# Optimization experiments

Measured on AMD Instinct MI355X. Metric: run time of the kernel, lower is better.

The kernel has to match this reference:

```python
import jax, jax.numpy as jnp
import numpy as np

EMBED = 1024
HEADS = 16
HEAD_DIM = EMBED // HEADS


def setup_inputs() -> dict:
    key = jax.random.key(0)
    ks = jax.random.split(key, 12)
    B, S, E = 2, 2048, EMBED
    scale = 1.0 / np.sqrt(E)
    inp = {
        "query": jax.random.normal(ks[0], (B, S, E), jnp.float32),
        "key": jax.random.normal(ks[1], (B, S, E), jnp.float32),
        "value": jax.random.normal(ks[2], (B, S, E), jnp.float32),
        "Wq": jax.random.normal(ks[3], (E, E), jnp.float32) * scale,
        "bq": jax.random.normal(ks[4], (E,), jnp.float32) * 0.01,
        "Wk": jax.random.normal(ks[5], (E, E), jnp.float32) * scale,
        "bk": jax.random.normal(ks[6], (E,), jnp.float32) * 0.01,
        "Wv": jax.random.normal(ks[7], (E, E), jnp.float32) * scale,
        "bv": jax.random.normal(ks[8], (E,), jnp.float32) * 0.01,
        "Wo": jax.random.normal(ks[9], (E, E), jnp.float32) * scale,
        "bo": jax.random.normal(ks[10], (E,), jnp.float32) * 0.01,
    }
    return inp


def reference(query, key, value, Wq, bq, Wk, bk, Wv, bv, Wo, bo):
    B, Sq, E = query.shape
    Sk = key.shape[1]
    H, D = HEADS, HEAD_DIM
    # QKV projections (torch Linear: x @ W.T + b)
    q = (query @ Wq.T + bq).reshape(B, Sq, H, D)
    k = (key @ Wk.T + bk).reshape(B, Sk, H, D)
    v = (value @ Wv.T + bv).reshape(B, Sk, H, D)
    # energy: [B, H, Sq, Sk]; note scale = 1/sqrt(embed_size), not head_dim
    energy = jnp.einsum("bqhd,bkhd->bhqk", q, k)
    scale = jnp.asarray(E, energy.dtype) ** 0.5
    attn = jax.nn.softmax(energy / scale, axis=-1)
    out = jnp.einsum("bhqk,bkhd->bqhd", attn, v).reshape(B, Sq, E)
    # fc_out (dropout is identity at eval)
    return out @ Wo.T + bo
```

## Files before the change

### kernel.cpp

```cpp
#include <hip/hip_runtime.h>
#include <hip/hip_bf16.h>

typedef __hip_bfloat16 bf16;
typedef short frag8 __attribute__((ext_vector_type(8)));
typedef _Float16 half4 __attribute__((ext_vector_type(4)));
typedef _Float16 half8 __attribute__((ext_vector_type(8)));
typedef __fp16 fp16x2 __attribute__((ext_vector_type(2)));
typedef float f32x4 __attribute__((ext_vector_type(4)));

typedef __attribute__((address_space(3))) void lds_void;
typedef __attribute__((address_space(1))) const void gbl_void;

__device__ __forceinline__ void gld16(const void* g, void* l) {
  __builtin_amdgcn_global_load_lds((gbl_void*)g, (lds_void*)l, 16, 0, 0);
}

__device__ __forceinline__ unsigned short f2bf(float f) {
  union { float f; unsigned u; } x; x.f = f;
  unsigned r = x.u + 0x7FFFu + ((x.u >> 16) & 1u);
  return (unsigned short)(r >> 16);
}

#define QSCALE 0.0450842200278f
#define MFIX 4.0f

struct CvtArgs {
  const float4* src[7];
  ushort4* dst[7];
  int n4[7];
};
__global__ __launch_bounds__(256) void cvt_all(CvtArgs a) {
  const int t = blockIdx.y;
  const int i = blockIdx.x * 256 + threadIdx.x;
  if (i >= a.n4[t]) return;
  float4 v = a.src[t][i];
  ushort4 o;
  o.x = f2bf(v.x); o.y = f2bf(v.y); o.z = f2bf(v.z); o.w = f2bf(v.w);
  a.dst[t][i] = o;
}

__device__ __forceinline__ void mfma32(f32x4 (&acc)[8][4], const frag8 (&a8)[8], const frag8 (&b4)[4]) {
  __builtin_amdgcn_s_setprio(1);
  #pragma unroll
  for (int i = 0; i < 8; ++i) {
    #pragma unroll
    for (int j = 0; j < 4; ++j)
      acc[i][j] = __builtin_amdgcn_mfma_f32_16x16x32_bf16(a8[i], b4[j], acc[i][j], 0, 0, 0);
  }
  __builtin_amdgcn_s_setprio(0);
}

__global__ __launch_bounds__(512, 2)
void gemm_qkv256(const bf16* __restrict__ A0, const bf16* __restrict__ A1, const bf16* __restrict__ A2,
                 const bf16* __restrict__ W0, const bf16* __restrict__ W1, const bf16* __restrict__ W2,
                 const float* __restrict__ b0, const float* __restrict__ b1, const float* __restrict__ b2,
                 void* __restrict__ o0, void* __restrict__ o1, void* __restrict__ o2) {
  __shared__ __align__(16) char smem[131072];
  bf16* As = (bf16*)smem;
  bf16* Bs = (bf16*)(smem + 65536);
  const int tid = threadIdx.x;
  const int wave = tid >> 6, lane = tid & 63, quad = lane >> 4, l16 = lane & 15;
  const int wm = wave >> 2, wn = wave & 3;
  const int bn = blockIdx.x, bm = blockIdx.y, z = blockIdx.z;

  const bf16* A = A0; const bf16* W = W0; const float* bias = b0; void* out = o0;
  if (z == 1) { A = A1; W = W1; bias = b1; out = o1; }
  else if (z == 2) { A = A2; W = W2; bias = b2; out = o2; }

  const bf16* Ab = A + (size_t)bm * 256 * 1024;
  const bf16* Wb = W + (size_t)bn * 256 * 1024;
  const int c0_ = tid & 3, r0_ = tid >> 2;
  const int gcp = ((c0_ ^ ((r0_ >> 1) & 3)) << 3);
  const int rc2 = (quad ^ ((l16 >> 1) & 3)) << 3;

  auto stageA = [&](int kt, bf16* dst) {
    #pragma unroll
    for (int is = 0; is < 2; ++is) {
      const int r = r0_ + is * 128;
      gld16(Ab + (size_t)r * 1024 + kt * 32 + gcp, (void*)(dst + (is * 512 + tid) * 8));
    }
  };
  auto stageW = [&](int kt, bf16* dst) {
    #pragma unroll
    for (int is = 0; is < 2; ++is) {
      const int r = r0_ + is * 128;
      gld16(Wb + (size_t)r * 1024 + kt * 32 + gcp, (void*)(dst + (is * 512 + tid) * 8));
    }
  };
  auto ldsA8 = [&](const bf16* ah, frag8 (&a8)[8]) {
    #pragma unroll
    for (int i = 0; i < 8; ++i)
      a8[i] = *(const frag8*)&ah[(wm * 128 + i * 16 + l16) * 32 + rc2];
  };
  auto ldsB4 = [&](const bf16* bh, frag8 (&b4)[4]) {
    #pragma unroll
    for (int j = 0; j < 4; ++j)
      b4[j] = *(const frag8*)&bh[(wn * 64 + j * 16 + l16) * 32 + rc2];
  };

  f32x4 acc[8][4];
  #pragma unroll
  for (int i = 0; i < 8; ++i)
    #pragma unroll
    for (int j = 0; j < 4; ++j)
      acc[i][j] = (f32x4){0.f, 0.f, 0.f, 0.f};

  stageA(0, As + 0 * 8192); stageW(0, Bs + 0 * 8192);
  stageA(1, As + 1 * 8192); stageW(1, Bs + 1 * 8192);
  stageA(2, As + 2 * 8192); stageW(2, Bs + 2 * 8192);

  #pragma unroll 4
  for (int t = 0; t < 28; ++t) {
    asm volatile("s_waitcnt vmcnt(8)" ::: "memory");
    __builtin_amdgcn_s_barrier();
    const bf16* ab = As + (t & 3) * 8192;
    const bf16* bb = Bs + (t & 3) * 8192;
    frag8 a8[8], b4[4];
    ldsA8(ab, a8); ldsB4(bb, b4);
    stageA(t + 3, As + ((t + 3) & 3) * 8192);
    stageW(t + 3, Bs + ((t + 3) & 3) * 8192);
    asm volatile("s_waitcnt lgkmcnt(0)" ::: "memory");
    mfma32(acc, a8, b4);
  }
  {
    asm volatile("s_waitcnt vmcnt(8)" ::: "memory");
    __builtin_amdgcn_s_barrier();
    frag8 a8[8], b4[4];
    ldsA8(As + 0 * 8192, a8); ldsB4(Bs + 0 * 8192, b4);
    stageA(31, As + 3 * 8192);
    stageW(31, Bs + 3 * 8192);
    asm volatile("s_waitcnt lgkmcnt(0)" ::: "memory");
    mfma32(acc, a8, b4);
  }
  {
    asm volatile("s_waitcnt vmcnt(8)" ::: "memory");
    __builtin_amdgcn_s_barrier();
    frag8 a8[8], b4[4];
    ldsA8(As + 1 * 8192, a8); ldsB4(Bs + 1 * 8192, b4);
    asm volatile("s_waitcnt lgkmcnt(0)" ::: "memory");
    mfma32(acc, a8, b4);
  }
  {
    asm volatile("s_waitcnt vmcnt(4)" ::: "memory");
    __builtin_amdgcn_s_barrier();
    frag8 a8[8], b4[4];
    ldsA8(As + 2 * 8192, a8); ldsB4(Bs + 2 * 8192, b4);
    asm volatile("s_waitcnt lgkmcnt(0)" ::: "memory");
    mfma32(acc, a8, b4);
  }
  {
    asm volatile("s_waitcnt vmcnt(0)" ::: "memory");
    __builtin_amdgcn_s_barrier();
    frag8 a8[8], b4[4];
    ldsA8(As + 3 * 8192, a8); ldsB4(Bs + 3 * 8192, b4);
    asm volatile("s_waitcnt lgkmcnt(0)" ::: "memory");
    mfma32(acc, a8, b4);
  }

  if (z == 2) {
    _Float16* vlds = (_Float16*)smem;
    __builtin_amdgcn_s_barrier();
    #pragma unroll
    for (int j = 0; j < 4; ++j) {
      const int col = bn * 256 + wn * 64 + j * 16 + l16;
      const float bv = bias[col];
      const int d = j * 16 + l16;
      #pragma unroll
      for (int i = 0; i < 8; ++i) {
        const int g = wm * 2 + (i >> 2);
        const int kb = (i & 3) * 16 + quad * 4;
        half4 h;
        #pragma unroll
        for (int r = 0; r < 4; ++r)
          h[r] = (_Float16)(acc[i][j][r] + bv);
        const int off = ((wn * 4 + g) << 12) + d * 64 + ((((kb >> 3) ^ (d & 7)) << 3)) + (kb & 7);
        *(half4*)&vlds[off] = h;
      }
    }
    __builtin_amdgcn_s_barrier();
    const int b_ = bm >> 3;
    #pragma unroll
    for (int rd = 0; rd < 16; ++rd) {
      const int l = rd * 4096 + tid * 8;
      const int wnp = l >> 14, g = (l >> 12) & 3, off = l & 4095;
      const size_t bhp = (size_t)(b_ * 16 + bn * 4 + wnp);
      const size_t addr = bhp * 131072 + (size_t)((bm & 7) * 4 + g) * 4096 + (size_t)off;
      *(uint4*)&((_Float16*)out)[addr] = *(const uint4*)&vlds[l];
    }
  } else {
    #pragma unroll
    for (int j = 0; j < 4; ++j) {
      const int col = bn * 256 + wn * 64 + j * 16 + l16;
      const float bv = bias[col];
      #pragma unroll
      for (int i = 0; i < 8; ++i) {
        #pragma unroll
        for (int r = 0; r < 4; ++r) {
          const int row = bm * 256 + wm * 128 + i * 16 + quad * 4 + r;
          float v = acc[i][j][r] + bv;
          const int b = row >> 11, s = row & 2047;
          const int hh = col >> 6, d = col & 63;
          const size_t bh = (size_t)(b * 16 + hh);
          if (z == 0) {
            v *= QSCALE;
            ((bf16*)out)[(bh * 2048 + s) * 64 + d] = __float2bfloat16(v);
          } else {
            const int g = s >> 6, l32 = s & 31, G32 = (s >> 5) & 1;
            const int q_ = (l32 >> 3) & 3, t_ = (l32 >> 2) & 1, i_ = l32 & 3;
            const int r64 = G32 * 32 + t_ * 16 + q_ * 4 + i_;
            const size_t addr = bh * 131072 + (size_t)g * 4096 + (size_t)r64 * 64
                              + (size_t)(((d >> 3) ^ (r64 & 7)) << 3) + (d & 7);
            ((bf16*)out)[addr] = __float2bfloat16(v);
          }
        }
      }
    }
  }
}

template<int MODE>
__global__ __launch_bounds__(256)
void gemm_bt(const bf16* __restrict__ A0, const bf16* __restrict__ A1, const bf16* __restrict__ A2,
             const bf16* __restrict__ W0, const bf16* __restrict__ W1, const bf16* __restrict__ W2,
             const float* __restrict__ b0, const float* __restrict__ b1, const float* __restrict__ b2,
             void* __restrict__ o0, void* __restrict__ o1, void* __restrict__ o2) {
  constexpr int NK = 1024;
  constexpr int BN = (MODE == 1) ? 128 : 64;
  __shared__ __align__(16) bf16 As[2][128 * 32];
  __shared__ __align__(16) bf16 Bs[2][BN * 32];
  const int tid = threadIdx.x;
  const int wave = tid >> 6, lane = tid & 63, quad = lane >> 4, l16 = lane & 15;
  const int wm = wave >> 1, wn = wave & 1;
  const int bn = blockIdx.x, bm = blockIdx.y;

  const bf16* A = A0; const bf16* W = W0; const float* bias = b0; void* out = o0;

  const bf16* Ab = A + (size_t)bm * 128 * NK;
  const bf16* Wb = W + (size_t)bn * BN * NK;
  const int c0_ = tid & 3, r0_ = tid >> 2;
  const int rc = (quad ^ (l16 & 3)) << 3;

  auto stageA = [&](int k0, int buf) {
    #pragma unroll
    for (int is = 0; is < 2; ++is) {
      const int c = tid + is * 256;
      const int r = r0_ + is * 64;
      const int gc = (c0_ ^ (r & 3)) << 3;
      gld16(Ab + (size_t)r * NK + k0 + gc, (void*)(&As[buf][(size_t)c * 8]));
    }
  };
  auto stageW = [&](int k0, int buf) {
    const int r = r0_;
    const int gc = (c0_ ^ (r & 3)) << 3;
    gld16(Wb + (size_t)r * NK + k0 + gc, (void*)(&Bs[buf][(size_t)tid * 8]));
  };

  f32x4 acc[4][2];
  #pragma unroll
  for (int i = 0; i < 4; ++i)
    #pragma unroll
    for (int j = 0; j < 2; ++j)
      acc[i][j] = (f32x4){0.f, 0.f, 0.f, 0.f};

  stageA(0, 0); stageW(0, 0);
  #pragma unroll 2
  for (int kt = 0; kt < 32; ++kt) {
    __syncthreads();
    if (kt < 31) { stageA((kt + 1) * 32, (kt + 1) & 1); stageW((kt + 1) * 32, (kt + 1) & 1); }
    const bf16* as_ = As[kt & 1];
    const bf16* bs_ = Bs[kt & 1];
    frag8 af[4], bfr[2];
    #pragma unroll
    for (int i = 0; i < 4; ++i)
      af[i] = *(const frag8*)&as_[(wm * 64 + i * 16 + l16) * 32 + rc];
    #pragma unroll
    for (int j = 0; j < 2; ++j)
      bfr[j] = *(const frag8*)&bs_[(wn * 32 + j * 16 + l16) * 32 + rc];
    #pragma unroll
    for (int i = 0; i < 4; ++i)
      #pragma unroll
      for (int j = 0; j < 2; ++j)
        acc[i][j] = __builtin_amdgcn_mfma_f32_16x16x32_bf16(af[i], bfr[j], acc[i][j], 0, 0, 0);
  }

  #pragma unroll
  for (int j = 0; j < 2; ++j) {
    const int col = bn * 64 + wn * 32 + j * 16 + l16;
    const float bv = bias[col];
    #pragma unroll
    for (int i = 0; i < 4; ++i) {
      #pragma unroll
      for (int r = 0; r < 4; ++r) {
        const int row = bm * 128 + wm * 64 + i * 16 + quad * 4 + r;
        ((float*)out)[(size_t)row * 1024 + col] = acc[i][j][r] + bv;
      }
    }
  }
}

__global__ __launch_bounds__(512, 2)
void flash_attn(const bf16* __restrict__ Q, const bf16* __restrict__ K,
                const _Float16* __restrict__ Vt, bf16* __restrict__ ctx) {
  __shared__ __align__(16) char smem[65536];
  bf16* Ks = (bf16*)smem;
  _Float16* Vs = (_Float16*)(smem + 32768);
  const int tid = threadIdx.x;
  const int wave = tid >> 6, lane = tid & 63, quad = lane >> 4, l16 = lane & 15;
  const int qg = wave & 3, kvg = wave >> 2;
  const int bh = blockIdx.x, b = bh >> 4, h = bh & 15;
  const int q0 = blockIdx.y * 256 + qg * 64;
  const bf16* Qb = Q + (size_t)bh * 131072;
  const bf16* Kb = K + (size_t)bh * 131072;
  const _Float16* Vb = Vt + (size_t)bh * 131072;

  frag8 qf[4][2];
  #pragma unroll
  for (int qt = 0; qt < 4; ++qt)
    #pragma unroll
    for (int ks = 0; ks < 2; ++ks)
      qf[qt][ks] = *(const frag8*)(Qb + (size_t)(q0 + qt * 16 + l16) * 64 + ks * 32 + quad * 8);

  f32x4 rsv[4];
  f32x4 o[4][4];
  #pragma unroll
  for (int qt = 0; qt < 4; ++qt) {
    rsv[qt] = (f32x4){0.f, 0.f, 0.f, 0.f};
    #pragma unroll
    for (int dt = 0; dt < 4; ++dt)
      o[qt][dt] = (f32x4){0.f, 0.f, 0.f, 0.f};
  }

  const int xk = l16 & 7;

  auto stage = [&](int kt, int buf) {
    #pragma unroll
    for (int s = 0; s < 2; ++s) {
      const int g = s * 16 + kt;
      gld16(Kb + (size_t)g * 4096 + (size_t)tid * 8, (void*)(Ks + (s * 2 + buf) * 4096 + tid * 8));
      gld16(Vb + (size_t)g * 4096 + (size_t)tid * 8, (void*)(Vs + (s * 2 + buf) * 4096 + tid * 8));
    }
  };

  stage(0, 0);
  #pragma unroll 2
  for (int kt = 0; kt < 16; ++kt) {
    __syncthreads();
    if (kt < 15) stage(kt + 1, (kt + 1) & 1);
    const bf16* ks_ = Ks + (kvg * 2 + (kt & 1)) * 4096;
    const _Float16* vs_ = Vs + (kvg * 2 + (kt & 1)) * 4096;

    f32x4 s[4][4];
    #pragma unroll
    for (int qt = 0; qt < 4; ++qt)
      #pragma unroll
      for (int jt = 0; jt < 4; ++jt)
        s[qt][jt] = (f32x4){-MFIX, -MFIX, -MFIX, -MFIX};
    #pragma unroll
    for (int ks = 0; ks < 2; ++ks) {
      frag8 kf[4];
      #pragma unroll
      for (int jt = 0; jt < 4; ++jt)
        kf[jt] = *(const frag8*)&ks_[(jt * 16 + l16) * 64 + (((ks * 4 + quad) ^ xk) << 3)];
      __builtin_amdgcn_s_setprio(1);
      #pragma unroll
      for (int qt = 0; qt < 4; ++qt)
        #pragma unroll
        for (int jt = 0; jt < 4; ++jt)
          s[qt][jt] = __builtin_amdgcn_mfma_f32_16x16x32_bf16(kf[jt], qf[qt][ks], s[qt][jt], 0, 0, 0);
      __builtin_amdgcn_s_setprio(0);
    }

    half8 pb[4][2];
    #pragma unroll
    for (int qt = 0; qt < 4; ++qt) {
      #pragma unroll
      for (int jt = 0; jt < 4; ++jt) {
        f32x4 p4;
        #pragma unroll
        for (int r = 0; r < 4; ++r)
          p4[r] = __builtin_amdgcn_exp2f(s[qt][jt][r]);
        rsv[qt] += p4;
        union { fp16x2 h2[2]; half4 h4; } u;
        u.h2[0] = __builtin_amdgcn_cvt_pkrtz(p4[0], p4[1]);
        u.h2[1] = __builtin_amdgcn_cvt_pkrtz(p4[2], p4[3]);
        const int jtp = jt >> 1, hi = (jt & 1) * 4;
        pb[qt][jtp][hi + 0] = u.h4[0];
        pb[qt][jtp][hi + 1] = u.h4[1];
        pb[qt][jtp][hi + 2] = u.h4[2];
        pb[qt][jtp][hi + 3] = u.h4[3];
      }
    }

    #pragma unroll
    for (int jtp = 0; jtp < 2; ++jtp) {
      half8 vf[4];
      #pragma unroll
      for (int dt = 0; dt < 4; ++dt)
        vf[dt] = *(const half8*)&vs_[(dt * 16 + l16) * 64 + (((jtp * 4 + quad) ^ xk) << 3)];
      __builtin_amdgcn_s_setprio(1);
      #pragma unroll
      for (int qt = 0; qt < 4; ++qt)
        #pragma unroll
        for (int dt = 0; dt < 4; ++dt)
          o[qt][dt] = __builtin_amdgcn_mfma_f32_16x16x32_f16(vf[dt], pb[qt][jtp], o[qt][dt], 0, 0, 0);
      __builtin_amdgcn_s_setprio(0);
    }
  }

  float4* mo = (float4*)smem;
  float*  ml = (float*)(smem + 32768);
  const int mbase = (qg * 64 + lane) * 8;
  #pragma unroll
  for (int r = 0; r < 2; ++r) {
    __syncthreads();
    if (kvg == 1) {
      #pragma unroll
      for (int qh = 0; qh < 2; ++qh) {
        const int qt = r * 2 + qh;
        #pragma unroll
        for (int dt = 0; dt < 4; ++dt) {
          const int i = qh * 4 + dt;
          mo[mbase + (i ^ (lane & 7))] = (float4){o[qt][dt][0], o[qt][dt][1], o[qt][dt][2], o[qt][dt][3]};
        }
        ml[(qg * 64 + lane) * 2 + qh] = rsv[qt][0] + rsv[qt][1] + rsv[qt][2] + rsv[qt][3];
      }
    }
    __syncthreads();
    if (kvg == 0) {
      #pragma unroll
      for (int qh = 0; qh < 2; ++qh) {
        const int qt = r * 2 + qh;
        float l = rsv[qt][0] + rsv[qt][1] + rsv[qt][2] + rsv[qt][3]
                + ml[(qg * 64 + lane) * 2 + qh];
        l += __shfl_xor(l, 16, 64);
        l += __shfl_xor(l, 32, 64);
        const float inv = __builtin_amdgcn_rcpf(l);
        const int q = q0 + qt * 16 + l16;
        #pragma unroll
        for (int dt = 0; dt < 4; ++dt) {
          const int i = qh * 4 + dt;
          const float4 po = mo[mbase + (i ^ (lane & 7))];
          ushort4 w;
          w.x = f2bf((o[qt][dt][0] + po.x) * inv);
          w.y = f2bf((o[qt][dt][1] + po.y) * inv);
          w.z = f2bf((o[qt][dt][2] + po.z) * inv);
          w.w = f2bf((o[qt][dt][3] + po.w) * inv);
          const int d = dt * 16 + quad * 4;
          *(uint2*)&ctx[((size_t)(b * 2048 + q)) * 1024 + h * 64 + d] = *(uint2*)&w;
        }
      }
    }
  }
}

extern "C" void kernel_launch(void* const* d_in, const int* in_sizes, int n_in,
                              void* d_out, int out_size, void* d_ws, size_t ws_size,
                              hipStream_t stream) {
  const float* q_in = (const float*)d_in[0];
  const float* k_in = (const float*)d_in[1];
  const float* v_in = (const float*)d_in[2];
  const float* Wq = (const float*)d_in[3];
  const float* bq = (const float*)d_in[4];
  const float* Wk = (const float*)d_in[5];
  const float* bk = (const float*)d_in[6];
  const float* Wv = (const float*)d_in[7];
  const float* bv = (const float*)d_in[8];
  const float* Wo = (const float*)d_in[9];
  const float* bo = (const float*)d_in[10];

  char* ws = (char*)d_ws;
  const size_t MB = 1024 * 1024;
  bf16* Xq  = (bf16*)(ws + 0 * MB);
  bf16* Xk  = (bf16*)(ws + 8 * MB);
  bf16* Xv  = (bf16*)(ws + 16 * MB);
  bf16* Wqb = (bf16*)(ws + 24 * MB);
  bf16* Wkb = (bf16*)(ws + 26 * MB);
  bf16* Wvb = (bf16*)(ws + 28 * MB);
  bf16* Wob = (bf16*)(ws + 30 * MB);
  bf16* Qw  = (bf16*)(ws + 32 * MB);
  bf16* Kw  = (bf16*)(ws + 40 * MB);
  _Float16* Vtw = (_Float16*)(ws + 48 * MB);
  bf16* Ctx = (bf16*)(ws + 56 * MB);

  {
    CvtArgs a;
    a.src[0] = (const float4*)q_in; a.dst[0] = (ushort4*)Xq;  a.n4[0] = 4194304 / 4;
    a.src[1] = (const float4*)k_in; a.dst[1] = (ushort4*)Xk;  a.n4[1] = 4194304 / 4;
    a.src[2] = (const float4*)v_in; a.dst[2] = (ushort4*)Xv;  a.n4[2] = 4194304 / 4;
    a.src[3] = (const float4*)Wq;   a.dst[3] = (ushort4*)Wqb; a.n4[3] = 1048576 / 4;
    a.src[4] = (const float4*)Wk;   a.dst[4] = (ushort4*)Wkb; a.n4[4] = 1048576 / 4;
    a.src[5] = (const float4*)Wv;   a.dst[5] = (ushort4*)Wvb; a.n4[5] = 1048576 / 4;
    a.src[6] = (const float4*)Wo;   a.dst[6] = (ushort4*)Wob; a.n4[6] = 1048576 / 4;
    cvt_all<<<dim3(4096, 7), 256, 0, stream>>>(a);
  }

  gemm_qkv256<<<dim3(4, 16, 3), 512, 0, stream>>>(Xq, Xk, Xv, Wqb, Wkb, Wvb,
                                                  bq, bk, bv, Qw, Kw, (bf16*)Vtw);
  flash_attn<<<dim3(32, 8), 512, 0, stream>>>(Qw, Kw, Vtw, Ctx);
  gemm_bt<0><<<dim3(16, 32), 256, 0, stream>>>(Ctx, nullptr, nullptr, Wob, nullptr, nullptr,
                                               bo, nullptr, nullptr, d_out, nullptr, nullptr);
}
```

Before: 212.9 us.

## Deepen output GEMM pipeline to 4 stages and load K directly in attention

Replaces the output projection GEMM with a dedicated kernel using a 4-buffer LDS ring, three tiles prefetched ahead, explicit vmcnt waits, raw barriers and MFMA priority, plus a new swizzle. In flash attention, K fragments are read straight from global memory instead of staged through LDS. This cuts LDS to 36 KB so the launch bound can ask for 4 blocks per CU. The aim is better latency hiding and occupancy. The risk is higher global-load latency on K, and register pressure from the higher occupancy target.

```diff
diff --git a/kernel.cpp b/kernel.cpp
--- a/kernel.cpp
+++ b/kernel.cpp
@@ -218,41 +218,42 @@
   }
 }
 
-template<int MODE>
-__global__ __launch_bounds__(256)
-void gemm_bt(const bf16* __restrict__ A0, const bf16* __restrict__ A1, const bf16* __restrict__ A2,
-             const bf16* __restrict__ W0, const bf16* __restrict__ W1, const bf16* __restrict__ W2,
-             const float* __restrict__ b0, const float* __restrict__ b1, const float* __restrict__ b2,
-             void* __restrict__ o0, void* __restrict__ o1, void* __restrict__ o2) {
-  constexpr int NK = 1024;
-  constexpr int BN = (MODE == 1) ? 128 : 64;
-  __shared__ __align__(16) bf16 As[2][128 * 32];
-  __shared__ __align__(16) bf16 Bs[2][BN * 32];
+__global__ __launch_bounds__(256, 3)
+void gemm_out(const bf16* __restrict__ A, const bf16* __restrict__ W,
+              const float* __restrict__ bias, float* __restrict__ out) {
+  __shared__ __align__(16) char smem[49152];
+  bf16* As = (bf16*)smem;
+  bf16* Bs = (bf16*)(smem + 32768);
   const int tid = threadIdx.x;
   const int wave = tid >> 6, lane = tid & 63, quad = lane >> 4, l16 = lane & 15;
   const int wm = wave >> 1, wn = wave & 1;
   const int bn = blockIdx.x, bm = blockIdx.y;
 
-  const bf16* A = A0; const bf16* W = W0; const float* bias = b0; void* out = o0;
-
-  const bf16* Ab = A + (size_t)bm * 128 * NK;
-  const bf16* Wb = W + (size_t)bn * BN * NK;
+  const bf16* Ab = A + (size_t)bm * 128 * 1024;
+  const bf16* Wb = W + (size_t)bn * 64 * 1024;
   const int c0_ = tid & 3, r0_ = tid >> 2;
-  const int rc = (quad ^ (l16 & 3)) << 3;
-
-  auto stageA = [&](int k0, int buf) {
+  const int gcp = ((c0_ ^ ((r0_ >> 1) & 3)) << 3);
+  const int rc2 = (quad ^ ((l16 >> 1) & 3)) << 3;
+
+  auto stageA = [&](int kt, bf16* dst) {
     #pragma unroll
     for (int is = 0; is < 2; ++is) {
-      const int c = tid + is * 256;
       const int r = r0_ + is * 64;
-      const int gc = (c0_ ^ (r & 3)) << 3;
-      gld16(Ab + (size_t)r * NK + k0 + gc, (void*)(&As[buf][(size_t)c * 8]));
-    }
-  };
-  auto stageW = [&](int k0, int buf) {
-    const int r = r0_;
-    const int gc = (c0_ ^ (r & 3)) << 3;
-    gld16(Wb + (size_t)r * NK + k0 + gc, (void*)(&Bs[buf][(size_t)tid * 8]));
+      gld16(Ab + (size_t)r * 1024 + kt * 32 + gcp, (void*)(dst + (is * 256 + tid) * 8));
+    }
+  };
+  auto stageW = [&](int kt, bf16* dst) {
+    gld16(Wb + (size_t)r0_ * 1024 + kt * 32 + gcp, (void*)(dst + tid * 8));
+  };
+  auto ldsA4 = [&](const bf16* ah, frag8 (&a4)[4]) {
+    #pragma unroll
+    for (int i = 0; i < 4; ++i)
+      a4[i] = *(const frag8*)&ah[(wm * 64 + i * 16 + l16) * 32 + rc2];
+  };
+  auto ldsB2 = [&](const bf16* bh, frag8 (&b2)[2]) {
+    #pragma unroll
+    for (int j = 0; j < 2; ++j)
+      b2[j] = *(const frag8*)&bh[(wn * 32 + j * 16 + l16) * 32 + rc2];
   };
 
   f32x4 acc[4][2];
@@ -262,25 +263,56 @@
     for (int j = 0; j < 2; ++j)
       acc[i][j] = (f32x4){0.f, 0.f, 0.f, 0.f};
 
-  stageA(0, 0); stageW(0, 0);
-  #pragma unroll 2
-  for (int kt = 0; kt < 32; ++kt) {
-    __syncthreads();
-    if (kt < 31) { stageA((kt + 1) * 32, (kt + 1) & 1); stageW((kt + 1) * 32, (kt + 1) & 1); }
-    const bf16* as_ = As[kt & 1];
-    const bf16* bs_ = Bs[kt & 1];
-    frag8 af[4], bfr[2];
+  stageA(0, As + 0 * 4096); stageW(0, Bs + 0 * 2048);
+  stageA(1, As + 1 * 4096); stageW(1, Bs + 1 * 2048);
+  stageA(2, As + 2 * 4096); stageW(2, Bs + 2 * 2048);
+
+  auto body = [&](const bf16* ab, const bf16* bb) {
+    frag8 a4[4], b2[2];
+    ldsA4(ab, a4); ldsB2(bb, b2);
+    asm volatile("s_waitcnt lgkmcnt(0)" ::: "memory");
+    __builtin_amdgcn_s_setprio(1);
     #pragma unroll
     for (int i = 0; i < 4; ++i)
-      af[i] = *(const frag8*)&as_[(wm * 64 + i * 16 + l16) * 32 + rc];
-    #pragma unroll
-    for (int j = 0; j < 2; ++j)
-      bfr[j] = *(const frag8*)&bs_[(wn * 32 + j * 16 + l16) * 32 + rc];
+      #pragma unroll
+      for (int j = 0; j < 2; ++j)
+        acc[i][j] = __builtin_amdgcn_mfma_f32_16x16x32_bf16(a4[i], b2[j], acc[i][j], 0, 0, 0);
+    __builtin_amdgcn_s_setprio(0);
+  };
+
+  #pragma unroll 4
+  for (int t = 0; t < 29; ++t) {
+    asm volatile("s_waitcnt vmcnt(6)" ::: "memory");
+    __builtin_amdgcn_s_barrier();
+    const bf16* ab = As + (t & 3) * 4096;
+    const bf16* bb = Bs + (t & 3) * 2048;
+    frag8 a4[4], b2[2];
+    ldsA4(ab, a4); ldsB2(bb, b2);
+    stageA(t + 3, As + ((t + 3) & 3) * 4096);
+    stageW(t + 3, Bs + ((t + 3) & 3) * 2048);
+    asm volatile("s_waitcnt lgkmcnt(0)" ::: "memory");
+    __builtin_amdgcn_s_setprio(1);
     #pragma unroll
     for (int i = 0; i < 4; ++i)
       #pragma unroll
       for (int j = 0; j < 2; ++j)
-        acc[i][j] = __builtin_amdgcn_mfma_f32_16x16x32_bf16(af[i], bfr[j], acc[i][j], 0, 0, 0);
+        acc[i][j] = __builtin_amdgcn_mfma_f32_16x16x32_bf16(a4[i], b2[j], acc[i][j], 0, 0, 0);
+    __builtin_amdgcn_s_setprio(0);
+  }
+  {
+    asm volatile("s_waitcnt vmcnt(6)" ::: "memory");
+    __builtin_amdgcn_s_barrier();
+    body(As + 1 * 4096, Bs + 1 * 2048);
+  }
+  {
+    asm volatile("s_waitcnt vmcnt(3)" ::: "memory");
+    __builtin_amdgcn_s_barrier();
+    body(As + 2 * 4096, Bs + 2 * 2048);
+  }
+  {
+    asm volatile("s_waitcnt vmcnt(0)" ::: "memory");
+    __builtin_amdgcn_s_barrier();
+    body(As + 3 * 4096, Bs + 3 * 2048);
   }
 
   #pragma unroll
@@ -292,18 +324,17 @@
       #pragma unroll
       for (int r = 0; r < 4; ++r) {
         const int row = bm * 128 + wm * 64 + i * 16 + quad * 4 + r;
-        ((float*)out)[(size_t)row * 1024 + col] = acc[i][j][r] + bv;
+        out[(size_t)row * 1024 + col] = acc[i][j][r] + bv;
       }
     }
   }
 }
 
-__global__ __launch_bounds__(512, 2)
+__global__ __launch_bounds__(512, 4)
 void flash_attn(const bf16* __restrict__ Q, const bf16* __restrict__ K,
                 const _Float16* __restrict__ Vt, bf16* __restrict__ ctx) {
-  __shared__ __align__(16) char smem[65536];
-  bf16* Ks = (bf16*)smem;
-  _Float16* Vs = (_Float16*)(smem + 32768);
+  __shared__ __align__(16) char smem[36864];
+  _Float16* Vs = (_Float16*)smem;
   const int tid = threadIdx.x;
   const int wave = tid >> 6, lane = tid & 63, quad = lane >> 4, l16 = lane & 15;
   const int qg = wave & 3, kvg = wave >> 2;
@@ -331,22 +362,29 @@
   }
 
   const int xk = l16 & 7;
-
-  auto stage = [&](int kt, int buf) {
+  const int koff0 = l16 * 64 + ((quad ^ xk) << 3);
+  const int koff1 = l16 * 64 + (((4 + quad) ^ xk) << 3);
+
+  auto stageV = [&](int kt, int buf) {
     #pragma unroll
     for (int s = 0; s < 2; ++s) {
       const int g = s * 16 + kt;
-      gld16(Kb + (size_t)g * 4096 + (size_t)tid * 8, (void*)(Ks + (s * 2 + buf) * 4096 + tid * 8));
       gld16(Vb + (size_t)g * 4096 + (size_t)tid * 8, (void*)(Vs + (s * 2 + buf) * 4096 + tid * 8));
     }
   };
 
-  stage(0, 0);
+  stageV(0, 0);
   #pragma unroll 2
   for (int kt = 0; kt < 16; ++kt) {
     __syncthreads();
-    if (kt < 15) stage(kt + 1, (kt + 1) & 1);
-    const bf16* ks_ = Ks + (kvg * 2 + (kt & 1)) * 4096;
+    const bf16* kg = Kb + (size_t)(kvg * 16 + kt) * 4096;
+    frag8 kf0[4], kf1[4];
+    #pragma unroll
+    for (int jt = 0; jt < 4; ++jt) {
+      kf0[jt] = *(const frag8*)&kg[jt * 1024 + koff0];
+      kf1[jt] = *(const frag8*)&kg[jt * 1024 + koff1];
+    }
+    if (kt < 15) stageV(kt + 1, (kt + 1) & 1);
     const _Float16* vs_ = Vs + (kvg * 2 + (kt & 1)) * 4096;
 
     f32x4 s[4][4];
@@ -355,20 +393,18 @@
       #pragma unroll
       for (int jt = 0; jt < 4; ++jt)
         s[qt][jt] = (f32x4){-MFIX, -MFIX, -MFIX, -MFIX};
-    #pragma unroll
-    for (int ks = 0; ks < 2; ++ks) {
-      frag8 kf[4];
+    __builtin_amdgcn_s_setprio(1);
+    #pragma unroll
+    for (int qt = 0; qt < 4; ++qt)
       #pragma unroll
       for (int jt = 0; jt < 4; ++jt)
-        kf[jt] = *(const frag8*)&ks_[(jt * 16 + l16) * 64 + (((ks * 4 + quad) ^ xk) << 3)];
-      __builtin_amdgcn_s_setprio(1);
-      #pragma unroll
-      for (int qt = 0; qt < 4; ++qt)
-        #pragma unroll
-        for (int jt = 0; jt < 4; ++jt)
-          s[qt][jt] = __builtin_amdgcn_mfma_f32_16x16x32_bf16(kf[jt], qf[qt][ks], s[qt][jt], 0, 0, 0);
-      __builtin_amdgcn_s_setprio(0);
-    }
+        s[qt][jt] = __builtin_amdgcn_mfma_f32_16x16x32_bf16(kf0[jt], qf[qt][0], s[qt][jt], 0, 0, 0);
+    #pragma unroll
+    for (int qt = 0; qt < 4; ++qt)
+      #pragma unroll
+      for (int jt = 0; jt < 4; ++jt)
+        s[qt][jt] = __builtin_amdgcn_mfma_f32_16x16x32_bf16(kf1[jt], qf[qt][1], s[qt][jt], 0, 0, 0);
+    __builtin_amdgcn_s_setprio(0);
 
     half8 pb[4][2];
     #pragma unroll
@@ -497,6 +533,5 @@
   gemm_qkv256<<<dim3(4, 16, 3), 512, 0, stream>>>(Xq, Xk, Xv, Wqb, Wkb, Wvb,
                                                   bq, bk, bv, Qw, Kw, (bf16*)Vtw);
   flash_attn<<<dim3(32, 8), 512, 0, stream>>>(Qw, Kw, Vtw, Ctx);
-  gemm_bt<0><<<dim3(16, 32), 256, 0, stream>>>(Ctx, nullptr, nullptr, Wob, nullptr, nullptr,
-                                               bo, nullptr, nullptr, d_out, nullptr, nullptr);
-}
+  gemm_out<<<dim3(16, 32), 256, 0, stream>>>(Ctx, Wob, bo, (float*)d_out);
+}
```

Result: slower. 440.7 us (+107.0%).
